# Performance work log

Hardware: AMD Instinct MI355X
Metric: run time of the kernel (lower is better)

The kernel has to match this reference:

```python
import jax, jax.numpy as jnp
import numpy as np

BEAM = 64
RANK = 32
VOCAB = 21128


def setup_inputs() -> dict:
    key = jax.random.key(0)
    k1, k2, k3, k4 = jax.random.split(key, 4)
    B, S, V = 16, 256, VOCAB
    emissions = jax.random.normal(k1, (B, S, V), jnp.float32)
    targets = jax.random.randint(k2, (B, S), 0, V)
    mask = jnp.ones((B, S), dtype=bool)
    E1 = jax.random.normal(k3, (V, RANK), jnp.float32) * 0.02
    E2 = jax.random.normal(k4, (V, RANK), jnp.float32) * 0.02
    return {"emissions": emissions, "targets": targets, "mask": mask, "E1": E1, "E2": E2}


def _crf_llh(emissions, targets, mask, E1, E2, beam=BEAM):
    B, S, V = emissions.shape
    maskf = mask.astype(emissions.dtype)

    # ---- numerator: score of the target path ----
    em = jnp.take_along_axis(emissions, targets[:, :, None], axis=2)[:, :, 0]  # [B,S]
    trans = jnp.sum(E1[targets[:, :-1]] * E2[targets[:, 1:]], axis=2)          # [B,S-1]
    scores = em.at[:, 1:].add(trans)
    numerator = jnp.sum(scores * maskf, axis=1)                                # [B]

    # ---- denominator: beam-approximated normalizer ----
    # force target token into the beam (scatter +inf, then topk indices)
    b_idx = jnp.arange(B)[:, None]
    s_idx = jnp.arange(S)[None, :]
    _em = emissions.at[b_idx, s_idx, targets].set(jnp.inf)
    _, beam_targets = jax.lax.top_k(_em, beam)                                 # [B,S,beam]
    beam_em = jnp.take_along_axis(emissions, beam_targets, axis=2)             # [B,S,beam]

    t1 = E1[beam_targets[:, :-1]]                                              # [B,S-1,beam,rank]
    t2 = E2[beam_targets[:, 1:]]                                               # [B,S-1,beam,rank]
    beam_trans = jnp.einsum('bsir,bsjr->bsij', t1, t2)                         # [B,S-1,beam,beam]

    score0 = beam_em[:, 0]                                                     # [B,beam]

    def step(score, x):
        trans_i, emit_i, m_i = x
        nxt = jax.scipy.special.logsumexp(score[:, :, None] + trans_i, axis=1) + emit_i
        score = jnp.where(m_i[:, None], nxt, score)
        return score, None

    xs = (jnp.swapaxes(beam_trans, 0, 1),          # [S-1,B,beam,beam]
          jnp.swapaxes(beam_em[:, 1:], 0, 1),      # [S-1,B,beam]
          jnp.swapaxes(mask[:, 1:], 0, 1))         # [S-1,B]
    score, _ = jax.lax.scan(step, score0, xs)
    denominator = jax.scipy.special.logsumexp(score, axis=1)                   # [B]

    llh = numerator - denominator
    return jnp.sum(llh)  # reduction='sum'


def reference(emissions, targets, mask, E1, E2):
    return _crf_llh(emissions, targets, mask, E1, E2)
```

## Files before the change

### kernel.cpp

```cpp
#include <hip/hip_runtime.h>
#include <stdint.h>

#define Bn 16
#define Sn 256
#define Vn 21128
#define NV4 5282
#define RANKn 32
#define BEAMn 64
#define HBINS 4096
#define CAPn 512
#define NSEG 32
#define SEGLEN 8
#define LOG2E 1.44269504088896340736f
#define LN2   0.69314718055994530942f

#define EXP2F(x) __builtin_amdgcn_exp2f(x)
#define LOG2F(x) __builtin_amdgcn_logf(x)

__device__ __forceinline__ unsigned f2o(unsigned b) {
    return (b & 0x80000000u) ? ~b : (b | 0x80000000u);
}
__device__ __forceinline__ float o2f(unsigned u) {
    unsigned b = (u & 0x80000000u) ? (u ^ 0x80000000u) : ~u;
    return __uint_as_float(b);
}
__device__ __forceinline__ float dot4(float4 a, float4 b) {
    return a.x * b.x + a.y * b.y + a.z * b.z + a.w * b.w;
}

__global__ __launch_bounds__(256) void topk_kernel(const float* __restrict__ emis,
                                                   const int* __restrict__ targets,
                                                   const int* __restrict__ mask,
                                                   const float* __restrict__ E1,
                                                   const float* __restrict__ E2,
                                                   int* __restrict__ beam_idx,
                                                   float* __restrict__ beam_val,
                                                   float* __restrict__ out) {
    const int row = blockIdx.x;
    const float* __restrict__ rowp = emis + (size_t)row * Vn;
    const int tgt = targets[row];
    __shared__ unsigned hist[HBINS];
    __shared__ unsigned csum[256];
    __shared__ unsigned cu[CAPn];
    __shared__ int      cix[CAPn];
    __shared__ int      selidx[BEAMn];
    __shared__ float    selval[BEAMn];
    __shared__ unsigned ccount;
    __shared__ int      binstar;
    __shared__ int      chunkc;
    __shared__ int      hastgt;
    __shared__ unsigned wcnt[4];
    const int t = threadIdx.x;
    if (t == 0) { ccount = 0; hastgt = 0; }

    const unsigned THRU = f2o(__float_as_uint(2.5f));
    uint4 vals[21];
    unsigned cntl = 0;
    #pragma unroll
    for (int it = 0; it < 21; ++it) {
        int v4 = t + it * 256;
        if (v4 < NV4) {
            const uint4 raw = ((const uint4*)rowp)[v4];
            uint4 u;
            u.x = f2o(raw.x); u.y = f2o(raw.y); u.z = f2o(raw.z); u.w = f2o(raw.w);
            vals[it] = u;
            cntl += (u.x > THRU) + (u.y > THRU) + (u.z > THRU) + (u.w > THRU);
        }
    }
    for (int off = 32; off; off >>= 1) cntl += __shfl_xor(cntl, off, 64);
    if ((t & 63) == 0) wcnt[t >> 6] = cntl;
    __syncthreads();
    const unsigned C0 = wcnt[0] + wcnt[1] + wcnt[2] + wcnt[3];

    if (C0 >= BEAMn && C0 <= CAPn) {
        #pragma unroll
        for (int it = 0; it < 21; ++it) {
            int v4 = t + it * 256;
            if (v4 < NV4) {
                uint4 u = vals[it];
                int bi = v4 * 4;
                if (u.x > THRU) { unsigned p = atomicAdd(&ccount, 1u); cu[p] = u.x; cix[p] = bi;     }
                if (u.y > THRU) { unsigned p = atomicAdd(&ccount, 1u); cu[p] = u.y; cix[p] = bi + 1; }
                if (u.z > THRU) { unsigned p = atomicAdd(&ccount, 1u); cu[p] = u.z; cix[p] = bi + 2; }
                if (u.w > THRU) { unsigned p = atomicAdd(&ccount, 1u); cu[p] = u.w; cix[p] = bi + 3; }
            }
        }
    } else {
        for (int i = t; i < HBINS; i += 256) hist[i] = 0;
        __syncthreads();
        #pragma unroll
        for (int it = 0; it < 21; ++it) {
            int v4 = t + it * 256;
            if (v4 < NV4) {
                uint4 u = vals[it];
                atomicAdd(&hist[u.x >> 20], 1u);
                atomicAdd(&hist[u.y >> 20], 1u);
                atomicAdd(&hist[u.z >> 20], 1u);
                atomicAdd(&hist[u.w >> 20], 1u);
            }
        }
        __syncthreads();
        unsigned cs = 0;
        #pragma unroll
        for (int i = 0; i < 16; ++i) cs += hist[t * 16 + i];
        csum[t] = cs;
        __syncthreads();
        for (int off = 1; off < 256; off <<= 1) {
            unsigned v = csum[t] + ((t + off < 256) ? csum[t + off] : 0u);
            __syncthreads();
            csum[t] = v;
            __syncthreads();
        }
        if (csum[t] >= BEAMn && (t == 255 || csum[t + 1] < BEAMn)) chunkc = t;
        __syncthreads();
        if (t == 0) {
            int tc = chunkc;
            unsigned acc = (tc == 255) ? 0u : csum[tc + 1];
            int bs = tc * 16;
            for (int b2 = tc * 16 + 15; b2 >= tc * 16; --b2) {
                acc += hist[b2];
                if (acc >= BEAMn) { bs = b2; break; }
            }
            binstar = bs;
        }
        __syncthreads();
        const unsigned bstar = (unsigned)binstar;
        #pragma unroll
        for (int it = 0; it < 21; ++it) {
            int v4 = t + it * 256;
            if (v4 < NV4) {
                uint4 u = vals[it];
                int bi = v4 * 4;
                if ((u.x >> 20) >= bstar) { unsigned p = atomicAdd(&ccount, 1u); if (p < CAPn) { cu[p] = u.x; cix[p] = bi;     } }
                if ((u.y >> 20) >= bstar) { unsigned p = atomicAdd(&ccount, 1u); if (p < CAPn) { cu[p] = u.y; cix[p] = bi + 1; } }
                if ((u.z >> 20) >= bstar) { unsigned p = atomicAdd(&ccount, 1u); if (p < CAPn) { cu[p] = u.z; cix[p] = bi + 2; } }
                if ((u.w >> 20) >= bstar) { unsigned p = atomicAdd(&ccount, 1u); if (p < CAPn) { cu[p] = u.w; cix[p] = bi + 3; } }
            }
        }
    }
    __syncthreads();
    const int C = (int)min(ccount, (unsigned)CAPn);
    for (int p = t; p < C; p += 256) {
        unsigned up = cu[p]; int ip = cix[p];
        int rank = 0;
        for (int q = 0; q < C; ++q) {
            unsigned uq = cu[q];
            rank += (uq > up) || (uq == up && cix[q] < ip);
        }
        if (rank < BEAMn) { selidx[rank] = ip; selval[rank] = o2f(up); }
    }
    __syncthreads();
    if (t < BEAMn && selidx[t] == tgt) hastgt = 1;
    __syncthreads();
    if (t == 0 && !hastgt) { selidx[BEAMn - 1] = tgt; selval[BEAMn - 1] = rowp[tgt]; }
    __syncthreads();
    if (t < BEAMn) {
        beam_idx[(size_t)row * BEAMn + t] = selidx[t];
        beam_val[(size_t)row * BEAMn + t] = selval[t];
    }
    if (t == 0) {
        const int s = row & (Sn - 1);
        float val = 0.f;
        if (mask[row]) {
            float em = rowp[tgt];
            float tr = 0.f;
            if (s > 0) {
                int pv = targets[row - 1];
                const float4* p1 = (const float4*)(E1 + (size_t)pv * RANKn);
                const float4* p2 = (const float4*)(E2 + (size_t)tgt * RANKn);
                #pragma unroll
                for (int r = 0; r < 8; ++r) tr += dot4(p1[r], p2[r]);
            }
            val = em + tr;
        }
        atomicAdd(out, val);
    }
}

#define TPAD 68
__global__ __launch_bounds__(256, 2) void segprod_kernel(const float* __restrict__ E1,
                                                         const float* __restrict__ E2,
                                                         const int* __restrict__ beam_idx,
                                                         const float* __restrict__ beam_val,
                                                         const int* __restrict__ mask,
                                                         float* __restrict__ segP,
                                                         float* __restrict__ segL) {
    const int blk = blockIdx.x;
    const int b = blk >> 5, s = blk & 31;
    const int k0 = s * SEGLEN;
    const int nk = min(SEGLEN, (Sn - 1) - k0);
    const float* __restrict__ bv  = beam_val + (size_t)b * Sn * BEAMn;
    const int* __restrict__ mk   = mask + (size_t)b * Sn;
    const int* __restrict__ bidx = beam_idx + (size_t)b * Sn * BEAMn;
    __shared__ float Qa[64][64], Qb[64][64];
    __shared__ float Mld[64][68];
    __shared__ float e1t[RANKn][TPAD];
    __shared__ float e2t[RANKn][TPAD];
    __shared__ float elog[SEGLEN][64];
    __shared__ int   mvec[SEGLEN];
    __shared__ float wred[4];
    const int t = threadIdx.x;
    const int ti = t & 15, tj = t >> 4;
    const int i0 = ti * 4, j0 = tj * 4;

    for (int x = t; x < 4096; x += 256)
        (&Qa[0][0])[x] = ((x >> 6) == (x & 63)) ? 1.f : 0.f;
    for (int x = t; x < nk * 64; x += 256)
        elog[x >> 6][x & 63] = bv[(size_t)(k0 + (x >> 6) + 1) * BEAMn + (x & 63)] * LOG2E;
    if (t < nk) mvec[t] = mk[k0 + t + 1];
    __syncthreads();

    float (*Qc)[64] = Qa, (*Qn)[64] = Qb;
    const int srow = t >> 2, sq = t & 3;
    for (int kk = 0; kk < nk; ++kk) {
        const int live = mvec[kk];
        if (live) {
            const int rb = sq * 8;
            int i1 = bidx[(size_t)(k0 + kk) * BEAMn + srow];
            const float4* s1 = (const float4*)(E1 + (size_t)i1 * RANKn) + sq * 2;
            float4 a0 = s1[0], a1 = s1[1];
            int i2 = bidx[(size_t)(k0 + kk + 1) * BEAMn + srow];
            const float4* s2 = (const float4*)(E2 + (size_t)i2 * RANKn) + sq * 2;
            float4 b0 = s2[0], b1 = s2[1];
            e1t[rb + 0][srow] = a0.x; e1t[rb + 1][srow] = a0.y; e1t[rb + 2][srow] = a0.z; e1t[rb + 3][srow] = a0.w;
            e1t[rb + 4][srow] = a1.x; e1t[rb + 5][srow] = a1.y; e1t[rb + 6][srow] = a1.z; e1t[rb + 7][srow] = a1.w;
            e2t[rb + 0][srow] = b0.x; e2t[rb + 1][srow] = b0.y; e2t[rb + 2][srow] = b0.z; e2t[rb + 3][srow] = b0.w;
            e2t[rb + 4][srow] = b1.x; e2t[rb + 5][srow] = b1.y; e2t[rb + 6][srow] = b1.z; e2t[rb + 7][srow] = b1.w;
        }
        __syncthreads();
        if (live) {
            float macc[4][4] = {};
            #pragma unroll
            for (int r = 0; r < RANKn; ++r) {
                float4 a  = *(const float4*)&e1t[r][i0];
                float4 bb = *(const float4*)&e2t[r][j0];
                macc[0][0] += a.x * bb.x; macc[0][1] += a.x * bb.y; macc[0][2] += a.x * bb.z; macc[0][3] += a.x * bb.w;
                macc[1][0] += a.y * bb.x; macc[1][1] += a.y * bb.y; macc[1][2] += a.y * bb.z; macc[1][3] += a.y * bb.w;
                macc[2][0] += a.z * bb.x; macc[2][1] += a.z * bb.y; macc[2][2] += a.z * bb.z; macc[2][3] += a.z * bb.w;
                macc[3][0] += a.w * bb.x; macc[3][1] += a.w * bb.y; macc[3][2] += a.w * bb.z; macc[3][3] += a.w * bb.w;
            }
            const float4 el = *(const float4*)&elog[kk][j0];
            #pragma unroll
            for (int ii = 0; ii < 4; ++ii) {
                float4 o = { EXP2F(macc[ii][0] * LOG2E + el.x), EXP2F(macc[ii][1] * LOG2E + el.y),
                             EXP2F(macc[ii][2] * LOG2E + el.z), EXP2F(macc[ii][3] * LOG2E + el.w) };
                *(float4*)&Mld[i0 + ii][j0] = o;
            }
        }
        __syncthreads();
        if (live) {
            float acc[4][4] = {};
            for (int r = 0; r < 64; ++r) {
                float4 a  = *(const float4*)&Qc[r][i0];
                float4 bb = *(const float4*)&Mld[r][j0];
                acc[0][0] += a.x * bb.x; acc[0][1] += a.x * bb.y; acc[0][2] += a.x * bb.z; acc[0][3] += a.x * bb.w;
                acc[1][0] += a.y * bb.x; acc[1][1] += a.y * bb.y; acc[1][2] += a.y * bb.z; acc[1][3] += a.y * bb.w;
                acc[2][0] += a.z * bb.x; acc[2][1] += a.z * bb.y; acc[2][2] += a.z * bb.z; acc[2][3] += a.z * bb.w;
                acc[3][0] += a.w * bb.x; acc[3][1] += a.w * bb.y; acc[3][2] += a.w * bb.z; acc[3][3] += a.w * bb.w;
            }
            #pragma unroll
            for (int jj = 0; jj < 4; ++jj) {
                float4 w = { acc[0][jj], acc[1][jj], acc[2][jj], acc[3][jj] };
                *(float4*)&Qn[j0 + jj][i0] = w;
            }
            float (*tmp)[64] = Qc; Qc = Qn; Qn = tmp;
        }
        __syncthreads();
    }
    float lm = 0.f;
    for (int x = t; x < 4096; x += 256) lm = fmaxf(lm, (&Qc[0][0])[x]);
    for (int off = 32; off; off >>= 1) lm = fmaxf(lm, __shfl_xor(lm, off, 64));
    if ((t & 63) == 0) wred[t >> 6] = lm;
    __syncthreads();
    const float m = fmaxf(fmaxf(wred[0], wred[1]), fmaxf(wred[2], wred[3]));
    const float inv = 1.f / m;
    float* op = segP + (size_t)blk * 4096;
    for (int x = t; x < 4096; x += 256) op[x] = (&Qc[0][0])[x] * inv;
    if (t == 0) segL[blk] = LOG2F(m);
}

__global__ __launch_bounds__(256) void finale_kernel(const float* __restrict__ segP,
                                                     const float* __restrict__ segL,
                                                     const float* __restrict__ beam_val,
                                                     float* __restrict__ out) {
    const int b = blockIdx.x;
    const int t = threadIdx.x;
    const int w = t >> 6, j = t & 63;
    const float* __restrict__ bv = beam_val + (size_t)b * Sn * BEAMn;
    __shared__ float us[BEAMn];
    __shared__ float part[4][BEAMn + 1];
    float sc = bv[j] * LOG2E;
    float mx = sc;
    for (int off = 32; off; off >>= 1) mx = fmaxf(mx, __shfl_xor(mx, off, 64));
    float u = EXP2F(sc - mx);
    float Ltot = mx;
    const float* p0 = segP + ((size_t)b * NSEG) * 4096 + (size_t)j * 64 + w * 16;
    float4 ra0 = ((const float4*)p0)[0], ra1 = ((const float4*)p0)[1],
           ra2 = ((const float4*)p0)[2], ra3 = ((const float4*)p0)[3];
    for (int s2 = 0; s2 < NSEG; ++s2) {
        float4 rb0, rb1, rb2, rb3;
        if (s2 + 1 < NSEG) {
            const float* pn = segP + ((size_t)b * NSEG + s2 + 1) * 4096 + (size_t)j * 64 + w * 16;
            rb0 = ((const float4*)pn)[0]; rb1 = ((const float4*)pn)[1];
            rb2 = ((const float4*)pn)[2]; rb3 = ((const float4*)pn)[3];
        }
        if (w == 0) us[j] = u;
        __syncthreads();
        const float4* uu = (const float4*)&us[w * 16];
        float a2 = dot4(ra0, uu[0]) + dot4(ra1, uu[1]) + dot4(ra2, uu[2]) + dot4(ra3, uu[3]);
        part[w][j] = a2;
        __syncthreads();
        float tot = part[0][j] + part[1][j] + part[2][j] + part[3][j];
        float m = tot;
        for (int off = 32; off; off >>= 1) m = fmaxf(m, __shfl_xor(m, off, 64));
        u = tot / m;
        Ltot += LOG2F(m) + segL[b * NSEG + s2];
        ra0 = rb0; ra1 = rb1; ra2 = rb2; ra3 = rb3;
    }
    if (t < BEAMn) {
        float e = u;
        for (int off = 32; off; off >>= 1) e += __shfl_xor(e, off, 64);
        if (t == 0) atomicAdd(out, -LN2 * (Ltot + LOG2F(e)));
    }
}

extern "C" void kernel_launch(void* const* d_in, const int* in_sizes, int n_in,
                              void* d_out, int out_size, void* d_ws, size_t ws_size,
                              hipStream_t stream) {
    const float* emis    = (const float*)d_in[0];
    const int*   targets = (const int*)d_in[1];
    const int*   mask    = (const int*)d_in[2];
    const float* E1      = (const float*)d_in[3];
    const float* E2      = (const float*)d_in[4];
    float* out = (float*)d_out;
    char* ws = (char*)d_ws;
    int*   beam_idx = (int*)ws;
    float* beam_val = (float*)(ws + (1 << 20));
    float* segP     = (float*)(ws + (2 << 20));
    float* segL     = (float*)(ws + (10 << 20));

    (void)hipMemsetAsync(out, 0, sizeof(float), stream);
    hipLaunchKernelGGL(topk_kernel, dim3(Bn * Sn), dim3(256), 0, stream,
                       emis, targets, mask, E1, E2, beam_idx, beam_val, out);
    hipLaunchKernelGGL(segprod_kernel, dim3(Bn * NSEG), dim3(256), 0, stream,
                       E1, E2, beam_idx, beam_val, mask, segP, segL);
    hipLaunchKernelGGL(finale_kernel, dim3(Bn), dim3(256), 0, stream,
                       segP, segL, beam_val, out);
}
```

Baseline: 567.7 us.

## Fuse segment product and finale via cooperative grid sync; skip identity matmul

Merges the segment-product and finale kernels into one cooperative launch separated by a grid-wide barrier, removing a kernel launch boundary. It also skips the first 64x64 matrix product in each segment, since the starting matrix is the identity, and writes the exponentiated transition block straight into Q instead. A fallback to the two separate kernels remains if the cooperative launch fails. The grid sync makes 496 blocks wait on the slowest segment and requires all 512 blocks to be co-resident. The shared-memory footprint now includes the finale buffers.

```diff
diff --git a/kernel.cpp b/kernel.cpp
--- a/kernel.cpp
+++ b/kernel.cpp
@@ -1,5 +1,8 @@
 #include <hip/hip_runtime.h>
+#include <hip/hip_cooperative_groups.h>
 #include <stdint.h>
+
+namespace cg = cooperative_groups;
 
 #define Bn 16
 #define Sn 256
@@ -178,42 +181,46 @@
 }
 
 #define TPAD 68
-__global__ __launch_bounds__(256, 2) void segprod_kernel(const float* __restrict__ E1,
-                                                         const float* __restrict__ E2,
-                                                         const int* __restrict__ beam_idx,
-                                                         const float* __restrict__ beam_val,
-                                                         const int* __restrict__ mask,
-                                                         float* __restrict__ segP,
-                                                         float* __restrict__ segL) {
-    const int blk = blockIdx.x;
+struct SegSmem {
+    float Qa[64][64], Qb[64][64];
+    float Mld[64][68];
+    float e1t[RANKn][TPAD], e2t[RANKn][TPAD];
+    float elog[SEGLEN][64];
+    int   mvec[SEGLEN];
+    float wred[4];
+};
+struct FinSmem {
+    float us[BEAMn];
+    float part[4][BEAMn + 1];
+};
+
+__device__ __forceinline__ void segprod_body(SegSmem& sm, const int blk,
+        const float* __restrict__ E1, const float* __restrict__ E2,
+        const int* __restrict__ beam_idx, const float* __restrict__ beam_val,
+        const int* __restrict__ mask, float* __restrict__ segP,
+        float* __restrict__ segL) {
     const int b = blk >> 5, s = blk & 31;
     const int k0 = s * SEGLEN;
     const int nk = min(SEGLEN, (Sn - 1) - k0);
     const float* __restrict__ bv  = beam_val + (size_t)b * Sn * BEAMn;
     const int* __restrict__ mk   = mask + (size_t)b * Sn;
     const int* __restrict__ bidx = beam_idx + (size_t)b * Sn * BEAMn;
-    __shared__ float Qa[64][64], Qb[64][64];
-    __shared__ float Mld[64][68];
-    __shared__ float e1t[RANKn][TPAD];
-    __shared__ float e2t[RANKn][TPAD];
-    __shared__ float elog[SEGLEN][64];
-    __shared__ int   mvec[SEGLEN];
-    __shared__ float wred[4];
     const int t = threadIdx.x;
     const int ti = t & 15, tj = t >> 4;
     const int i0 = ti * 4, j0 = tj * 4;
 
     for (int x = t; x < 4096; x += 256)
-        (&Qa[0][0])[x] = ((x >> 6) == (x & 63)) ? 1.f : 0.f;
+        (&sm.Qa[0][0])[x] = ((x >> 6) == (x & 63)) ? 1.f : 0.f;
     for (int x = t; x < nk * 64; x += 256)
-        elog[x >> 6][x & 63] = bv[(size_t)(k0 + (x >> 6) + 1) * BEAMn + (x & 63)] * LOG2E;
-    if (t < nk) mvec[t] = mk[k0 + t + 1];
-    __syncthreads();
-
-    float (*Qc)[64] = Qa, (*Qn)[64] = Qb;
+        sm.elog[x >> 6][x & 63] = bv[(size_t)(k0 + (x >> 6) + 1) * BEAMn + (x & 63)] * LOG2E;
+    if (t < nk) sm.mvec[t] = mk[k0 + t + 1];
+    __syncthreads();
+
+    float (*Qc)[64] = sm.Qa, (*Qn)[64] = sm.Qb;
+    bool qempty = true;
     const int srow = t >> 2, sq = t & 3;
     for (int kk = 0; kk < nk; ++kk) {
-        const int live = mvec[kk];
+        const int live = sm.mvec[kk];
         if (live) {
             const int rb = sq * 8;
             int i1 = bidx[(size_t)(k0 + kk) * BEAMn + srow];
@@ -222,73 +229,88 @@
             int i2 = bidx[(size_t)(k0 + kk + 1) * BEAMn + srow];
             const float4* s2 = (const float4*)(E2 + (size_t)i2 * RANKn) + sq * 2;
             float4 b0 = s2[0], b1 = s2[1];
-            e1t[rb + 0][srow] = a0.x; e1t[rb + 1][srow] = a0.y; e1t[rb + 2][srow] = a0.z; e1t[rb + 3][srow] = a0.w;
-            e1t[rb + 4][srow] = a1.x; e1t[rb + 5][srow] = a1.y; e1t[rb + 6][srow] = a1.z; e1t[rb + 7][srow] = a1.w;
-            e2t[rb + 0][srow] = b0.x; e2t[rb + 1][srow] = b0.y; e2t[rb + 2][srow] = b0.z; e2t[rb + 3][srow] = b0.w;
-            e2t[rb + 4][srow] = b1.x; e2t[rb + 5][srow] = b1.y; e2t[rb + 6][srow] = b1.z; e2t[rb + 7][srow] = b1.w;
+            sm.e1t[rb + 0][srow] = a0.x; sm.e1t[rb + 1][srow] = a0.y; sm.e1t[rb + 2][srow] = a0.z; sm.e1t[rb + 3][srow] = a0.w;
+            sm.e1t[rb + 4][srow] = a1.x; sm.e1t[rb + 5][srow] = a1.y; sm.e1t[rb + 6][srow] = a1.z; sm.e1t[rb + 7][srow] = a1.w;
+            sm.e2t[rb + 0][srow] = b0.x; sm.e2t[rb + 1][srow] = b0.y; sm.e2t[rb + 2][srow] = b0.z; sm.e2t[rb + 3][srow] = b0.w;
+            sm.e2t[rb + 4][srow] = b1.x; sm.e2t[rb + 5][srow] = b1.y; sm.e2t[rb + 6][srow] = b1.z; sm.e2t[rb + 7][srow] = b1.w;
         }
         __syncthreads();
         if (live) {
             float macc[4][4] = {};
             #pragma unroll
             for (int r = 0; r < RANKn; ++r) {
-                float4 a  = *(const float4*)&e1t[r][i0];
-                float4 bb = *(const float4*)&e2t[r][j0];
+                float4 a  = *(const float4*)&sm.e1t[r][i0];
+                float4 bb = *(const float4*)&sm.e2t[r][j0];
                 macc[0][0] += a.x * bb.x; macc[0][1] += a.x * bb.y; macc[0][2] += a.x * bb.z; macc[0][3] += a.x * bb.w;
                 macc[1][0] += a.y * bb.x; macc[1][1] += a.y * bb.y; macc[1][2] += a.y * bb.z; macc[1][3] += a.y * bb.w;
                 macc[2][0] += a.z * bb.x; macc[2][1] += a.z * bb.y; macc[2][2] += a.z * bb.z; macc[2][3] += a.z * bb.w;
                 macc[3][0] += a.w * bb.x; macc[3][1] += a.w * bb.y; macc[3][2] += a.w * bb.z; macc[3][3] += a.w * bb.w;
             }
-            const float4 el = *(const float4*)&elog[kk][j0];
+            const float4 el = *(const float4*)&sm.elog[kk][j0];
+            float4 ex[4];
             #pragma unroll
             for (int ii = 0; ii < 4; ++ii) {
-                float4 o = { EXP2F(macc[ii][0] * LOG2E + el.x), EXP2F(macc[ii][1] * LOG2E + el.y),
-                             EXP2F(macc[ii][2] * LOG2E + el.z), EXP2F(macc[ii][3] * LOG2E + el.w) };
-                *(float4*)&Mld[i0 + ii][j0] = o;
+                ex[ii].x = EXP2F(macc[ii][0] * LOG2E + el.x);
+                ex[ii].y = EXP2F(macc[ii][1] * LOG2E + el.y);
+                ex[ii].z = EXP2F(macc[ii][2] * LOG2E + el.z);
+                ex[ii].w = EXP2F(macc[ii][3] * LOG2E + el.w);
+            }
+            if (qempty) {
+                float4 w0 = { ex[0].x, ex[1].x, ex[2].x, ex[3].x };
+                float4 w1 = { ex[0].y, ex[1].y, ex[2].y, ex[3].y };
+                float4 w2 = { ex[0].z, ex[1].z, ex[2].z, ex[3].z };
+                float4 w3 = { ex[0].w, ex[1].w, ex[2].w, ex[3].w };
+                *(float4*)&Qn[j0 + 0][i0] = w0;
+                *(float4*)&Qn[j0 + 1][i0] = w1;
+                *(float4*)&Qn[j0 + 2][i0] = w2;
+                *(float4*)&Qn[j0 + 3][i0] = w3;
+            } else {
+                #pragma unroll
+                for (int ii = 0; ii < 4; ++ii)
+                    *(float4*)&sm.Mld[i0 + ii][j0] = ex[ii];
             }
         }
         __syncthreads();
         if (live) {
-            float acc[4][4] = {};
-            for (int r = 0; r < 64; ++r) {
-                float4 a  = *(const float4*)&Qc[r][i0];
-                float4 bb = *(const float4*)&Mld[r][j0];
-                acc[0][0] += a.x * bb.x; acc[0][1] += a.x * bb.y; acc[0][2] += a.x * bb.z; acc[0][3] += a.x * bb.w;
-                acc[1][0] += a.y * bb.x; acc[1][1] += a.y * bb.y; acc[1][2] += a.y * bb.z; acc[1][3] += a.y * bb.w;
-                acc[2][0] += a.z * bb.x; acc[2][1] += a.z * bb.y; acc[2][2] += a.z * bb.z; acc[2][3] += a.z * bb.w;
-                acc[3][0] += a.w * bb.x; acc[3][1] += a.w * bb.y; acc[3][2] += a.w * bb.z; acc[3][3] += a.w * bb.w;
-            }
-            #pragma unroll
-            for (int jj = 0; jj < 4; ++jj) {
-                float4 w = { acc[0][jj], acc[1][jj], acc[2][jj], acc[3][jj] };
-                *(float4*)&Qn[j0 + jj][i0] = w;
+            if (!qempty) {
+                float acc[4][4] = {};
+                for (int r = 0; r < 64; ++r) {
+                    float4 a  = *(const float4*)&Qc[r][i0];
+                    float4 bb = *(const float4*)&sm.Mld[r][j0];
+                    acc[0][0] += a.x * bb.x; acc[0][1] += a.x * bb.y; acc[0][2] += a.x * bb.z; acc[0][3] += a.x * bb.w;
+                    acc[1][0] += a.y * bb.x; acc[1][1] += a.y * bb.y; acc[1][2] += a.y * bb.z; acc[1][3] += a.y * bb.w;
+                    acc[2][0] += a.z * bb.x; acc[2][1] += a.z * bb.y; acc[2][2] += a.z * bb.z; acc[2][3] += a.z * bb.w;
+                    acc[3][0] += a.w * bb.x; acc[3][1] += a.w * bb.y; acc[3][2] += a.w * bb.z; acc[3][3] += a.w * bb.w;
+                }
+                #pragma unroll
+                for (int jj = 0; jj < 4; ++jj) {
+                    float4 w = { acc[0][jj], acc[1][jj], acc[2][jj], acc[3][jj] };
+                    *(float4*)&Qn[j0 + jj][i0] = w;
+                }
             }
             float (*tmp)[64] = Qc; Qc = Qn; Qn = tmp;
+            qempty = false;
         }
         __syncthreads();
     }
     float lm = 0.f;
     for (int x = t; x < 4096; x += 256) lm = fmaxf(lm, (&Qc[0][0])[x]);
     for (int off = 32; off; off >>= 1) lm = fmaxf(lm, __shfl_xor(lm, off, 64));
-    if ((t & 63) == 0) wred[t >> 6] = lm;
-    __syncthreads();
-    const float m = fmaxf(fmaxf(wred[0], wred[1]), fmaxf(wred[2], wred[3]));
+    if ((t & 63) == 0) sm.wred[t >> 6] = lm;
+    __syncthreads();
+    const float m = fmaxf(fmaxf(sm.wred[0], sm.wred[1]), fmaxf(sm.wred[2], sm.wred[3]));
     const float inv = 1.f / m;
     float* op = segP + (size_t)blk * 4096;
     for (int x = t; x < 4096; x += 256) op[x] = (&Qc[0][0])[x] * inv;
     if (t == 0) segL[blk] = LOG2F(m);
 }
 
-__global__ __launch_bounds__(256) void finale_kernel(const float* __restrict__ segP,
-                                                     const float* __restrict__ segL,
-                                                     const float* __restrict__ beam_val,
-                                                     float* __restrict__ out) {
-    const int b = blockIdx.x;
+__device__ __forceinline__ void finale_body(FinSmem& fm, const int b,
+        const float* __restrict__ segP, const float* __restrict__ segL,
+        const float* __restrict__ beam_val, float* __restrict__ out) {
     const int t = threadIdx.x;
     const int w = t >> 6, j = t & 63;
     const float* __restrict__ bv = beam_val + (size_t)b * Sn * BEAMn;
-    __shared__ float us[BEAMn];
-    __shared__ float part[4][BEAMn + 1];
     float sc = bv[j] * LOG2E;
     float mx = sc;
     for (int off = 32; off; off >>= 1) mx = fmaxf(mx, __shfl_xor(mx, off, 64));
@@ -304,13 +326,13 @@
             rb0 = ((const float4*)pn)[0]; rb1 = ((const float4*)pn)[1];
             rb2 = ((const float4*)pn)[2]; rb3 = ((const float4*)pn)[3];
         }
-        if (w == 0) us[j] = u;
-        __syncthreads();
-        const float4* uu = (const float4*)&us[w * 16];
+        if (w == 0) fm.us[j] = u;
+        __syncthreads();
+        const float4* uu = (const float4*)&fm.us[w * 16];
         float a2 = dot4(ra0, uu[0]) + dot4(ra1, uu[1]) + dot4(ra2, uu[2]) + dot4(ra3, uu[3]);
-        part[w][j] = a2;
-        __syncthreads();
-        float tot = part[0][j] + part[1][j] + part[2][j] + part[3][j];
+        fm.part[w][j] = a2;
+        __syncthreads();
+        float tot = fm.part[0][j] + fm.part[1][j] + fm.part[2][j] + fm.part[3][j];
         float m = tot;
         for (int off = 32; off; off >>= 1) m = fmaxf(m, __shfl_xor(m, off, 64));
         u = tot / m;
@@ -322,6 +344,41 @@
         for (int off = 32; off; off >>= 1) e += __shfl_xor(e, off, 64);
         if (t == 0) atomicAdd(out, -LN2 * (Ltot + LOG2F(e)));
     }
+}
+
+__global__ __launch_bounds__(256, 2) void segfin_kernel(const float* __restrict__ E1,
+                                                        const float* __restrict__ E2,
+                                                        const int* __restrict__ beam_idx,
+                                                        const float* __restrict__ beam_val,
+                                                        const int* __restrict__ mask,
+                                                        float* __restrict__ segP,
+                                                        float* __restrict__ segL,
+                                                        float* __restrict__ out) {
+    __shared__ SegSmem sm;
+    __shared__ FinSmem fm;
+    segprod_body(sm, blockIdx.x, E1, E2, beam_idx, beam_val, mask, segP, segL);
+    cg::this_grid().sync();
+    if (blockIdx.x < Bn)
+        finale_body(fm, blockIdx.x, segP, segL, beam_val, out);
+}
+
+__global__ __launch_bounds__(256, 2) void segprod_kernel(const float* __restrict__ E1,
+                                                         const float* __restrict__ E2,
+                                                         const int* __restrict__ beam_idx,
+                                                         const float* __restrict__ beam_val,
+                                                         const int* __restrict__ mask,
+                                                         float* __restrict__ segP,
+                                                         float* __restrict__ segL) {
+    __shared__ SegSmem sm;
+    segprod_body(sm, blockIdx.x, E1, E2, beam_idx, beam_val, mask, segP, segL);
+}
+
+__global__ __launch_bounds__(256) void finale_kernel(const float* __restrict__ segP,
+                                                     const float* __restrict__ segL,
+                                                     const float* __restrict__ beam_val,
+                                                     float* __restrict__ out) {
+    __shared__ FinSmem fm;
+    finale_body(fm, blockIdx.x, segP, segL, beam_val, out);
 }
 
 extern "C" void kernel_launch(void* const* d_in, const int* in_sizes, int n_in,
@@ -342,8 +399,15 @@
     (void)hipMemsetAsync(out, 0, sizeof(float), stream);
     hipLaunchKernelGGL(topk_kernel, dim3(Bn * Sn), dim3(256), 0, stream,
                        emis, targets, mask, E1, E2, beam_idx, beam_val, out);
-    hipLaunchKernelGGL(segprod_kernel, dim3(Bn * NSEG), dim3(256), 0, stream,
-                       E1, E2, beam_idx, beam_val, mask, segP, segL);
-    hipLaunchKernelGGL(finale_kernel, dim3(Bn), dim3(256), 0, stream,
-                       segP, segL, beam_val, out);
-}
+
+    void* kargs[] = { (void*)&E1, (void*)&E2, (void*)&beam_idx, (void*)&beam_val,
+                      (void*)&mask, (void*)&segP, (void*)&segL, (void*)&out };
+    hipError_t ce = hipLaunchCooperativeKernel(reinterpret_cast<void*>(segfin_kernel),
+                                               dim3(Bn * NSEG), dim3(256), kargs, 0, stream);
+    if (ce != hipSuccess) {
+        hipLaunchKernelGGL(segprod_kernel, dim3(Bn * NSEG), dim3(256), 0, stream,
+                           E1, E2, beam_idx, beam_val, mask, segP, segL);
+        hipLaunchKernelGGL(finale_kernel, dim3(Bn), dim3(256), 0, stream,
+                           segP, segL, beam_val, out);
+    }
+}
```

Result: slower. 646.2 us (+13.8%).
